# Kernel tuning notes

Measured on AMD Instinct MI355X. Metric: run time of the kernel, lower is better.

## Reference

```python
import jax, jax.numpy as jnp
import numpy as np

D_MODEL = 1024
N_LAYER = 2
VOCAB = 32000
D_STATE = 16
D_INNER = 2048  # expand * d_model
DT_RANK = 64    # ceil(d_model / 16)
D_CONV = 4
B, L = 2, 1024


def setup_inputs() -> dict:
    key = jax.random.key(0)
    ks = jax.random.split(key, 8)
    s = lambda k, shape, scale=0.02: (jax.random.normal(k, shape, jnp.float32) * scale)
    return {
        "input_ids": jax.random.randint(ks[0], (B, L), 0, VOCAB),
        "emb": s(ks[1], (VOCAB, D_MODEL)),
        "norm_f_w": jnp.ones((D_MODEL,), jnp.float32),
        "W_in_l": s(ks[2], (N_LAYER, D_INNER, D_MODEL)),
        "W_in_r": s(ks[3], (N_LAYER, D_INNER, D_MODEL)),
        "conv_w": s(ks[4], (N_LAYER, D_INNER, D_CONV), 0.1),
        "conv_b": jnp.zeros((N_LAYER, D_INNER), jnp.float32),
        "W_x": s(ks[5], (N_LAYER, DT_RANK + 2 * D_STATE, D_INNER)),
        "W_dt": s(ks[6], (N_LAYER, D_INNER, DT_RANK)),
        "A_log": jnp.log(jnp.broadcast_to(jnp.arange(1, D_STATE + 1, dtype=jnp.float32), (N_LAYER, D_INNER, D_STATE))),
        "Dp": jnp.ones((N_LAYER, D_INNER), jnp.float32),
        "W_out": s(ks[7], (N_LAYER, D_MODEL, D_INNER)),
        "norm_w": jnp.ones((N_LAYER, D_MODEL), jnp.float32),
    }


def _rmsnorm(x, w, eps=1e-5):
    return x * jax.lax.rsqrt(jnp.mean(x * x, axis=-1, keepdims=True) + eps) * w


def _silu(x):
    return x * jax.nn.sigmoid(x)


def _selective_scan(u, delta, A, Bm, Cm, Dv):
    # u, delta: [b,l,d]; A: [d,n]; Bm, Cm: [b,l,n]; Dv: [d]
    deltaA = jnp.exp(jnp.einsum('bld,dn->bldn', delta, A))          # [b,l,d,n]
    deltaB_u = (delta * u)[..., None] * Bm[:, :, None, :]            # [b,l,d,n]

    def step(carry, inp):
        dA_t, dBu_t, C_t = inp                 # [b,d,n],[b,d,n],[b,n]
        x = dA_t * carry + dBu_t
        y = jnp.einsum('bdn,bn->bd', x, C_t)
        return x, y

    b, l, d = u.shape
    n = A.shape[1]
    x0 = jnp.zeros((b, d, n), u.dtype)
    xs = (jnp.swapaxes(deltaA, 0, 1), jnp.swapaxes(deltaB_u, 0, 1), jnp.swapaxes(Cm, 0, 1))
    _, ys = jax.lax.scan(step, x0, xs)         # ys: [l,b,d]
    return jnp.swapaxes(ys, 0, 1) + u * Dv


def _mamba_block(x, Wl, Wr, cw, cb, Wx, Wdt, Alog, Dv, Wo):
    b, l, _ = x.shape
    res = x @ Wr.T                              # [b,l,di]
    xi = x @ Wl.T                               # [b,l,di]
    # depthwise causal conv over length (torch pads d_conv-1 both sides then slices [:l])
    xt = jnp.swapaxes(xi, 1, 2)                 # [b,di,l]
    xc = jax.lax.conv_general_dilated(
        xt, cw[:, None, :], window_strides=(1,), padding=[(D_CONV - 1, 0)],
        dimension_numbers=('NCH', 'OIH', 'NCH'), feature_group_count=D_INNER)
    xc = xc + cb[None, :, None]
    u = _silu(jnp.swapaxes(xc, 1, 2))           # [b,l,di]
    x_dbl = u @ Wx.T                            # [b,l,dt_rank+2n]
    dlt = x_dbl[..., :DT_RANK]
    Bm = x_dbl[..., DT_RANK:DT_RANK + D_STATE]
    Cm = x_dbl[..., DT_RANK + D_STATE:]
    delta = jax.nn.softplus(dlt @ Wdt.T)        # [b,l,di]
    A = -jnp.exp(Alog)
    y = _selective_scan(u, delta, A, Bm, Cm, Dv)
    y = y * _silu(res)
    return y @ Wo.T


def reference(input_ids, emb, norm_f_w, W_in_l, W_in_r, conv_w, conv_b, W_x, W_dt, A_log, Dp, W_out, norm_w):
    x = emb[input_ids]                          # [b,l,d_model]
    for i in range(N_LAYER):
        x = _mamba_block(_rmsnorm(x, norm_w[i]), W_in_l[i], W_in_r[i], conv_w[i], conv_b[i],
                         W_x[i], W_dt[i], A_log[i], Dp[i], W_out[i]) + x
    x = _rmsnorm(x, norm_f_w)
    return x @ emb.T                            # tied lm_head: [b,l,vocab]
```

## Files before the change

### kernel.cpp

```cpp
#include <hip/hip_runtime.h>
#include <math.h>

#define D_MODEL 1024
#define N_LAYER 2
#define VOCAB   32000
#define D_STATE 16
#define D_INNER 2048
#define DT_RANK 64
#define D_CONV  4
#define BB      2
#define LL      1024
#define TT      (BB*LL)
#define XLD     (2*D_INNER)

typedef __attribute__((ext_vector_type(8))) short bf16x8;
typedef __attribute__((ext_vector_type(4))) float f32x4;

static __device__ __forceinline__ unsigned short bfr(float f) {
  unsigned int u = __float_as_uint(f);
  return (unsigned short)((u + 0x7FFFu + ((u >> 16) & 1u)) >> 16);
}
static __device__ __forceinline__ float b2f(unsigned short h) {
  return __uint_as_float((unsigned int)h << 16);
}
static __device__ __forceinline__ unsigned int pack2(float a, float b) {
  return (unsigned int)bfr(a) | ((unsigned int)bfr(b) << 16);
}

template<int CTRL>
static __device__ __forceinline__ float dpp_sum_step(float x) {
  int v = __builtin_amdgcn_update_dpp(0, __float_as_int(x), CTRL, 0xF, 0xF, false);
  return x + __int_as_float(v);
}

static __device__ __forceinline__ void gload16(const void* g, void* l) {
  __builtin_amdgcn_global_load_lds(
      (const __attribute__((address_space(1))) void*)g,
      (__attribute__((address_space(3))) void*)l, 16, 0, 0);
}

__global__ __launch_bounds__(256) void embed_kernel(
    const int* __restrict__ ids, const float* __restrict__ emb,
    float* __restrict__ x) {
  int t  = blockIdx.x;
  int id = ids[t];
  const float4* src = (const float4*)(emb + (size_t)id * D_MODEL);
  float4*       dst = (float4*)(x + (size_t)t * D_MODEL);
  dst[threadIdx.x] = src[threadIdx.x];
}

__global__ __launch_bounds__(256) void rmsnorm_bf_kernel(
    const float* __restrict__ x, const float* __restrict__ w,
    unsigned short* __restrict__ o) {
  int t = blockIdx.x;
  const float4* xr = (const float4*)(x + (size_t)t * D_MODEL);
  float4 v = xr[threadIdx.x];
  float ss = v.x*v.x + v.y*v.y + v.z*v.z + v.w*v.w;
  for (int off = 32; off > 0; off >>= 1) ss += __shfl_down(ss, off, 64);
  __shared__ float wsum[4];
  if ((threadIdx.x & 63) == 0) wsum[threadIdx.x >> 6] = ss;
  __syncthreads();
  float tot = wsum[0] + wsum[1] + wsum[2] + wsum[3];
  float scale = rsqrtf(tot / (float)D_MODEL + 1e-5f);
  float4 wv = ((const float4*)w)[threadIdx.x];
  ushort4 ov;
  ov.x = bfr(v.x * scale * wv.x);
  ov.y = bfr(v.y * scale * wv.y);
  ov.z = bfr(v.z * scale * wv.z);
  ov.w = bfr(v.w * scale * wv.w);
  ((ushort4*)(o + (size_t)t * D_MODEL))[threadIdx.x] = ov;
}

__global__ __launch_bounds__(256) void cvt_bf_kernel(
    const float* __restrict__ s, unsigned short* __restrict__ d, int n8) {
  int i = blockIdx.x * 256 + threadIdx.x;
  if (i >= n8) return;
  const float4* p = (const float4*)s + (size_t)i * 2;
  float4 a = p[0], b = p[1];
  uint4 o;
  o.x = pack2(a.x, a.y); o.y = pack2(a.z, a.w);
  o.z = pack2(b.x, b.y); o.w = pack2(b.z, b.w);
  ((uint4*)d)[i] = o;
}

__global__ __launch_bounds__(256) void cvt_dlt_kernel(
    const float* __restrict__ xdbl, unsigned short* __restrict__ d) {
  int i = blockIdx.x * 256 + threadIdx.x;
  int t = i >> 3, j8 = (i & 7) * 8;
  const float4* p = (const float4*)(xdbl + (size_t)t * 128 + j8);
  float4 a = p[0], b = p[1];
  uint4 o;
  o.x = pack2(a.x, a.y); o.y = pack2(a.z, a.w);
  o.z = pack2(b.x, b.y); o.w = pack2(b.z, b.w);
  *(uint4*)(d + (size_t)t * 64 + j8) = o;
}

__global__ __launch_bounds__(256) void zero_kernel(float* __restrict__ p) {
  ((float4*)p)[blockIdx.x * 256 + threadIdx.x] = make_float4(0.f, 0.f, 0.f, 0.f);
}

#define GBM 128
#define GBN 128
#define GBK 32
#define LDK 40

template<bool BF>
static __device__ __forceinline__ void stage8(short* dst, const void* src, int ld,
                                              int grow, int gcol, bool valid) {
  uint4 w = make_uint4(0u, 0u, 0u, 0u);
  if (valid) {
    if constexpr (BF) {
      w = *(const uint4*)((const unsigned short*)src + (size_t)grow * ld + gcol);
    } else {
      const float* p = (const float*)src + (size_t)grow * ld + gcol;
      float4 v0 = *(const float4*)p;
      float4 v1 = *(const float4*)(p + 4);
      w.x = pack2(v0.x, v0.y); w.y = pack2(v0.z, v0.w);
      w.z = pack2(v1.x, v1.y); w.w = pack2(v1.z, v1.w);
    }
  }
  *(uint4*)dst = w;
}

template<bool ABF, bool BBF, bool RESID>
__global__ __launch_bounds__(256) void gemm_mfma(
    const void* __restrict__ Av, int lda,
    const void* __restrict__ Bv, int ldb,
    float* __restrict__ C, int ldc,
    int N, int K, const float* __restrict__ resid) {
  __shared__ short As[GBM * LDK];
  __shared__ short Bs[GBN * LDK];
  const int tid  = threadIdx.x;
  const int lane = tid & 63;
  const int wid  = tid >> 6;
  const int wm   = (wid >> 1) * 64;
  const int wn   = (wid & 1) * 64;
  const int bm   = blockIdx.y * GBM;
  const int bn   = blockIdx.x * GBN;

  f32x4 acc[4][4] = {};

  const int r0 = tid >> 2;
  const int cg = (tid & 3) * 8;
  const int fm = wm + (lane & 15);
  const int fn = wn + (lane & 15);
  const int fk = (lane >> 4) * 8;

  for (int k0 = 0; k0 < K; k0 += GBK) {
    stage8<ABF>(&As[(size_t)r0 * LDK + cg],        Av, lda, bm + r0,      k0 + cg, true);
    stage8<ABF>(&As[(size_t)(r0 + 64) * LDK + cg], Av, lda, bm + r0 + 64, k0 + cg, true);
    stage8<BBF>(&Bs[(size_t)r0 * LDK + cg],        Bv, ldb, bn + r0,      k0 + cg, (bn + r0) < N);
    stage8<BBF>(&Bs[(size_t)(r0 + 64) * LDK + cg], Bv, ldb, bn + r0 + 64, k0 + cg, (bn + r0 + 64) < N);
    __syncthreads();

    bf16x8 aq[4], bq[4];
#pragma unroll
    for (int i = 0; i < 4; i++) aq[i] = *(const bf16x8*)&As[(size_t)(fm + 16 * i) * LDK + fk];
#pragma unroll
    for (int i = 0; i < 4; i++) bq[i] = *(const bf16x8*)&Bs[(size_t)(fn + 16 * i) * LDK + fk];
#pragma unroll
    for (int mt = 0; mt < 4; mt++)
#pragma unroll
      for (int nt = 0; nt < 4; nt++)
        acc[mt][nt] = __builtin_amdgcn_mfma_f32_16x16x32_bf16(
            aq[mt], bq[nt], acc[mt][nt], 0, 0, 0);
    __syncthreads();
  }

  const int col   = lane & 15;
  const int rbase = (lane >> 4) * 4;
#pragma unroll
  for (int mt = 0; mt < 4; mt++) {
#pragma unroll
    for (int nt = 0; nt < 4; nt++) {
      int gn = bn + wn + nt * 16 + col;
      if (gn < N) {
        int gm = bm + wm + mt * 16 + rbase;
#pragma unroll
        for (int i = 0; i < 4; i++) {
          size_t o = (size_t)(gm + i) * ldc + gn;
          float r = RESID ? resid[o] : 0.f;
          C[o] = acc[mt][nt][i] + r;
        }
      }
    }
  }
}

#define NBM 128
#define NBN 128
#define NBK 64

template<bool ATOMIC>
__global__ __launch_bounds__(256) void gemm_bf(
    const unsigned short* __restrict__ A, int lda,
    const unsigned short* __restrict__ B, int ldb,
    float* __restrict__ C, int ldc,
    int N, int kc, int gx, int nwg) {
  __shared__ short As[NBM * NBK];
  __shared__ short Bs[NBN * NBK];
  const int tid  = threadIdx.x;
  const int lane = tid & 63;
  const int wid  = tid >> 6;
  const int wm   = (wid >> 1) * 64;
  const int wn   = (wid & 1) * 64;

  const int lin = blockIdx.y * gx + blockIdx.x;
  const int swz = (lin & 7) * (nwg >> 3) + (lin >> 3);
  const int bm  = (swz % gx) * NBM;
  const int bn  = (swz / gx) * NBN;
  const int kb  = blockIdx.z * kc;

  const int sr  = tid >> 3;
  const int scl = 8 * ((tid & 7) ^ (sr & 7));
  const unsigned short* pA[4];
  const unsigned short* pB[4];
#pragma unroll
  for (int i = 0; i < 4; i++) {
    pA[i] = A + (size_t)(bm + sr + 32 * i) * lda + kb + scl;
    int rb = bn + sr + 32 * i; if (rb >= N) rb = N - 1;
    pB[i] = B + (size_t)rb * ldb + kb + scl;
  }
  short* lA = As + tid * 8;
  short* lB = Bs + tid * 8;

  f32x4 acc[4][4] = {};
  const int fr = lane & 15;
  const int fs = lane >> 4;

  for (int k0 = 0; k0 < kc; k0 += NBK) {
#pragma unroll
    for (int i = 0; i < 4; i++) gload16(pA[i], lA + i * 2048);
#pragma unroll
    for (int i = 0; i < 4; i++) gload16(pB[i], lB + i * 2048);
    __syncthreads();

    bf16x8 aq[2][4], bq[2][4];
#pragma unroll
    for (int kk = 0; kk < 2; kk++) {
#pragma unroll
      for (int i = 0; i < 4; i++) {
        int ra = wm + 16 * i + fr;
        aq[kk][i] = *(const bf16x8*)&As[ra * 64 + 8 * ((kk * 4 + fs) ^ (ra & 7))];
        int rb = wn + 16 * i + fr;
        bq[kk][i] = *(const bf16x8*)&Bs[rb * 64 + 8 * ((kk * 4 + fs) ^ (rb & 7))];
      }
    }
#pragma unroll
    for (int kk = 0; kk < 2; kk++)
#pragma unroll
      for (int mt = 0; mt < 4; mt++)
#pragma unroll
        for (int nt = 0; nt < 4; nt++)
          acc[mt][nt] = __builtin_amdgcn_mfma_f32_16x16x32_bf16(
              aq[kk][mt], bq[kk][nt], acc[mt][nt], 0, 0, 0);
    __syncthreads();
#pragma unroll
    for (int i = 0; i < 4; i++) { pA[i] += NBK; pB[i] += NBK; }
  }

  const int col   = lane & 15;
  const int rbase = (lane >> 4) * 4;
#pragma unroll
  for (int mt = 0; mt < 4; mt++) {
#pragma unroll
    for (int nt = 0; nt < 4; nt++) {
      int gn = bn + wn + nt * 16 + col;
      if (gn < N) {
        int gm = bm + wm + mt * 16 + rbase;
#pragma unroll
        for (int i = 0; i < 4; i++) {
          size_t o = (size_t)(gm + i) * ldc + gn;
          if constexpr (ATOMIC) atomicAdd(&C[o], acc[mt][nt][i]);
          else                  C[o] = acc[mt][nt][i];
        }
      }
    }
  }
}

__global__ __launch_bounds__(256) void conv_silu_kernel(
    const float* __restrict__ xires, const float* __restrict__ cw,
    const float* __restrict__ cb, unsigned short* __restrict__ u) {
  size_t idx = (size_t)blockIdx.x * 256 + threadIdx.x;
  int j = (int)(idx & (D_INNER - 1));
  int t = (int)(idx >> 11);
  int b = t >> 10;
  int l = t & (LL - 1);
  float acc = cb[j];
#pragma unroll
  for (int k = 0; k < D_CONV; k++) {
    int ls = l - (D_CONV - 1) + k;
    if (ls >= 0)
      acc += xires[((size_t)b * LL + ls) * XLD + j] * cw[j * D_CONV + k];
  }
  float sig = 1.f / (1.f + __expf(-acc));
  u[idx] = bfr(acc * sig);
}

#define CT 64
#define NC (LL / CT)

__global__ __launch_bounds__(256) void scan_kernel(
    const float* __restrict__ xires,
    const unsigned short* __restrict__ ub,
    const float* __restrict__ xdbl,
    const float* __restrict__ Alog,
    const float* __restrict__ Dp,
    unsigned short* __restrict__ yg) {
  const int tid = threadIdx.x;
  const int d0  = blockIdx.x * 16;
  const int b   = blockIdx.y;
  const int dl  = tid >> 4;
  const int n   = tid & 15;
  const int tq  = tid >> 2;
  const int jq  = tid & 3;

  __shared__ float4 sc[2][CT][17];
  __shared__ float2 bcs[2][CT][17];

  const float a = -__expf(Alog[(size_t)(d0 + dl) * D_STATE + n]);
  const float4 Dv4 = *(const float4*)(Dp + d0 + jq * 4);
  const float* Dvp = (const float*)&Dv4;

  const size_t bt = (size_t)b * LL;
  float st = 0.f;
  unsigned short* outp = yg + bt * D_INNER + d0 + dl;

  auto loadc = [&](int c, float4& xi4, float4& rs4, ushort4& u4,
                   float4& B4, float4& C4) {
    size_t r = bt + (size_t)c * CT + tq;
    const float* row = xires + r * XLD + d0 + jq * 4;
    xi4 = *(const float4*)row;
    rs4 = *(const float4*)(row + D_INNER);
    u4  = *(const ushort4*)(ub  + r * D_INNER + d0 + jq * 4);
    B4  = *(const float4*)(xdbl + r * 128 + 64 + jq * 4);
    C4  = *(const float4*)(xdbl + r * 128 + 80 + jq * 4);
  };
  auto xform = [&](int bw, float4 xi4, float4 rs4, ushort4 u4,
                   float4 B4, float4 C4) {
    const float* xp = (const float*)&xi4;
    const float* rp = (const float*)&rs4;
    const unsigned short* up = (const unsigned short*)&u4;
    const float* Bp = (const float*)&B4;
    const float* Cp = (const float*)&C4;
#pragma unroll
    for (int j = 0; j < 4; j++) {
      float dr = xp[j], rv = rp[j], uv = b2f(up[j]);
      float dlt = fmaxf(dr, 0.f) + log1pf(__expf(-fabsf(dr)));
      float g   = rv / (1.f + __expf(-rv));
      float4 s;
      s.x = dlt; s.y = dlt * uv; s.z = g; s.w = uv * Dvp[j] * g;
      sc[bw][tq][jq * 4 + j] = s;
      float2 w; w.x = Bp[j]; w.y = Cp[j];
      bcs[bw][tq][jq * 4 + j] = w;
    }
  };

  {
    float4 xi4, rs4, B4, C4; ushort4 u4;
    loadc(0, xi4, rs4, u4, B4, C4);
    xform(0, xi4, rs4, u4, B4, C4);
  }
  __syncthreads();

  int buf = 0;
  for (int c = 0; c < NC; c++) {
    float4 xi4, rs4, B4, C4; ushort4 u4;
    const bool pf = (c + 1 < NC);
    if (pf) loadc(c + 1, xi4, rs4, u4, B4, C4);

#pragma unroll 8
    for (int t = 0; t < CT; t++) {
      float4 s = sc[buf][t][dl];
      float2 w = bcs[buf][t][n];
      float e  = __expf(s.x * a);
      st = fmaf(e, st, s.y * w.x);
      float yp = st * w.y;
      yp = dpp_sum_step<0x111>(yp);
      yp = dpp_sum_step<0x112>(yp);
      yp = dpp_sum_step<0x114>(yp);
      yp = dpp_sum_step<0x118>(yp);
      if (n == 15)
        outp[(size_t)(c * CT + t) * D_INNER] = bfr(fmaf(yp, s.z, s.w));
    }

    if (pf) xform(buf ^ 1, xi4, rs4, u4, B4, C4);
    __syncthreads();
    buf ^= 1;
  }
}

extern "C" void kernel_launch(void* const* d_in, const int* in_sizes, int n_in,
                              void* d_out, int out_size, void* d_ws, size_t ws_size,
                              hipStream_t stream) {
  const int*   ids    = (const int*)  d_in[0];
  const float* emb    = (const float*)d_in[1];
  const float* normfw = (const float*)d_in[2];
  const float* Winl   = (const float*)d_in[3];
  const float* Winr   = (const float*)d_in[4];
  const float* convw  = (const float*)d_in[5];
  const float* convb  = (const float*)d_in[6];
  const float* Wx     = (const float*)d_in[7];
  const float* Wdt    = (const float*)d_in[8];
  const float* Alog   = (const float*)d_in[9];
  const float* Dp     = (const float*)d_in[10];
  const float* Wout   = (const float*)d_in[11];
  const float* normw  = (const float*)d_in[12];
  float* out = (float*)d_out;

  float* x    = (float*)d_ws;
  float* xi   = x    + (size_t)TT * D_MODEL;
  float* res  = xi   + (size_t)TT * D_INNER;
  float* xdbl = res  + (size_t)TT * D_INNER;
  unsigned short* xn_bf = (unsigned short*)(xdbl + (size_t)TT * 128);
  unsigned short* u_bf  = xn_bf + (size_t)TT * D_MODEL;
  unsigned short* yg_bf = u_bf  + (size_t)TT * D_INNER;
  unsigned short* dlt_bf = yg_bf  + (size_t)TT * D_INNER;
  unsigned short* emb_bf = dlt_bf + (size_t)TT * DT_RANK;
  unsigned short* wlr_bf = emb_bf + (size_t)VOCAB * D_MODEL;
  unsigned short* wx_bf  = wlr_bf + (size_t)N_LAYER * 2 * D_INNER * D_MODEL;
  unsigned short* wdt_bf = wx_bf  + (size_t)N_LAYER * (DT_RANK + 2*D_STATE) * D_INNER;
  unsigned short* wout_bf= wdt_bf + (size_t)N_LAYER * D_INNER * DT_RANK;
  const size_t NEED = (size_t)((char*)(wout_bf + (size_t)N_LAYER * D_MODEL * D_INNER) - (char*)d_ws);
  const bool big = ws_size >= NEED;

  float* xires = xi;

  embed_kernel<<<TT, 256, 0, stream>>>(ids, emb, x);

  if (big) {
    cvt_bf_kernel<<<(VOCAB*D_MODEL/8 + 255)/256, 256, 0, stream>>>(emb, emb_bf, VOCAB*D_MODEL/8);
    for (int i = 0; i < N_LAYER; i++) {
      unsigned short* dst = wlr_bf + (size_t)i * 2 * D_INNER * D_MODEL;
      cvt_bf_kernel<<<(D_INNER*D_MODEL/8 + 255)/256, 256, 0, stream>>>(
          Winl + (size_t)i * D_INNER * D_MODEL, dst, D_INNER*D_MODEL/8);
      cvt_bf_kernel<<<(D_INNER*D_MODEL/8 + 255)/256, 256, 0, stream>>>(
          Winr + (size_t)i * D_INNER * D_MODEL, dst + (size_t)D_INNER*D_MODEL, D_INNER*D_MODEL/8);
    }
    cvt_bf_kernel<<<(N_LAYER*96*D_INNER/8 + 255)/256, 256, 0, stream>>>(Wx, wx_bf, N_LAYER*96*D_INNER/8);
    cvt_bf_kernel<<<(N_LAYER*D_INNER*DT_RANK/8 + 255)/256, 256, 0, stream>>>(Wdt, wdt_bf, N_LAYER*D_INNER*DT_RANK/8);
    cvt_bf_kernel<<<(N_LAYER*D_MODEL*D_INNER/8 + 255)/256, 256, 0, stream>>>(Wout, wout_bf, N_LAYER*D_MODEL*D_INNER/8);

    for (int i = 0; i < N_LAYER; i++) {
      const unsigned short* wlr = wlr_bf + (size_t)i * 2 * D_INNER * D_MODEL;
      const unsigned short* wx  = wx_bf  + (size_t)i * 96 * D_INNER;
      const unsigned short* wdt = wdt_bf + (size_t)i * D_INNER * DT_RANK;
      const unsigned short* wo  = wout_bf+ (size_t)i * D_MODEL * D_INNER;
      const float* cw  = convw + (size_t)i * D_INNER * D_CONV;
      const float* cb  = convb + (size_t)i * D_INNER;
      const float* Al  = Alog  + (size_t)i * D_INNER * D_STATE;
      const float* Dpl = Dp    + (size_t)i * D_INNER;
      const float* nw  = normw + (size_t)i * D_MODEL;

      rmsnorm_bf_kernel<<<TT, 256, 0, stream>>>(x, nw, xn_bf);
      gemm_bf<false><<<dim3(TT/NBM, XLD/NBN), 256, 0, stream>>>(
          xn_bf, D_MODEL, wlr, D_MODEL, xires, XLD, XLD, D_MODEL,
          TT/NBM, (TT/NBM)*(XLD/NBN));
      conv_silu_kernel<<<(TT * D_INNER) / 256, 256, 0, stream>>>(xires, cw, cb, u_bf);
      zero_kernel<<<(TT * 128 / 4) / 256, 256, 0, stream>>>(xdbl);
      gemm_bf<true><<<dim3(TT/NBM, 1, 16), 256, 0, stream>>>(
          u_bf, D_INNER, wx, D_INNER, xdbl, 128, 96, D_INNER / 16,
          TT/NBM, TT/NBM);
      cvt_dlt_kernel<<<(TT * 8) / 256, 256, 0, stream>>>(xdbl, dlt_bf);
      gemm_bf<false><<<dim3(TT/NBM, D_INNER/NBN), 256, 0, stream>>>(
          dlt_bf, DT_RANK, wdt, DT_RANK, xires, XLD, D_INNER, DT_RANK,
          TT/NBM, (TT/NBM)*(D_INNER/NBN));
      scan_kernel<<<dim3(D_INNER/16, BB), 256, 0, stream>>>(
          xires, u_bf, xdbl, Al, Dpl, yg_bf);
      gemm_bf<true><<<dim3(TT/NBM, D_MODEL/NBN, 4), 256, 0, stream>>>(
          yg_bf, D_INNER, wo, D_INNER, x, D_MODEL, D_MODEL, D_INNER / 4,
          TT/NBM, (TT/NBM)*(D_MODEL/NBN));
    }

    rmsnorm_bf_kernel<<<TT, 256, 0, stream>>>(x, normfw, xn_bf);
    gemm_bf<false><<<dim3(TT/NBM, VOCAB/NBN), 256, 0, stream>>>(
        xn_bf, D_MODEL, emb_bf, D_MODEL, out, VOCAB, VOCAB, D_MODEL,
        TT/NBM, (TT/NBM)*(VOCAB/NBN));
    return;
  }

  for (int i = 0; i < N_LAYER; i++) {
    const float* Wl  = Winl  + (size_t)i * D_INNER * D_MODEL;
    const float* Wr  = Winr  + (size_t)i * D_INNER * D_MODEL;
    const float* cw  = convw + (size_t)i * D_INNER * D_CONV;
    const float* cb  = convb + (size_t)i * D_INNER;
    const float* Wxl = Wx    + (size_t)i * (DT_RANK + 2*D_STATE) * D_INNER;
    const float* Wdl = Wdt   + (size_t)i * D_INNER * DT_RANK;
    const float* Al  = Alog  + (size_t)i * D_INNER * D_STATE;
    const float* Dpl = Dp    + (size_t)i * D_INNER;
    const float* Wo  = Wout  + (size_t)i * D_MODEL * D_INNER;
    const float* nw  = normw + (size_t)i * D_MODEL;

    rmsnorm_bf_kernel<<<TT, 256, 0, stream>>>(x, nw, xn_bf);
    gemm_mfma<true, false, false><<<dim3(D_INNER/GBN, TT/GBM), 256, 0, stream>>>(
        xn_bf, D_MODEL, Wl, D_MODEL, xi, D_INNER, D_INNER, D_MODEL, nullptr);
    gemm_mfma<true, false, false><<<dim3(D_INNER/GBN, TT/GBM), 256, 0, stream>>>(
        xn_bf, D_MODEL, Wr, D_MODEL, res, D_INNER, D_INNER, D_MODEL, nullptr);
    {
    }
    conv_silu_kernel<<<(TT * D_INNER) / 256, 256, 0, stream>>>(
        xi, cw, cb, u_bf);
    gemm_mfma<true, false, false><<<dim3(1, TT/GBM), 256, 0, stream>>>(
        u_bf, D_INNER, Wxl, D_INNER, xdbl, 128, DT_RANK + 2*D_STATE, D_INNER, nullptr);
    gemm_mfma<false, false, false><<<dim3(D_INNER/GBN, TT/GBM), 256, 0, stream>>>(
        xdbl, 128, Wdl, DT_RANK, xi, D_INNER, D_INNER, DT_RANK, nullptr);
    scan_kernel<<<dim3(D_INNER/16, BB), 256, 0, stream>>>(
        xi, u_bf, xdbl, Al, Dpl, yg_bf);
    gemm_mfma<true, false, true><<<dim3(D_MODEL/GBN, TT/GBM), 256, 0, stream>>>(
        yg_bf, D_INNER, Wo, D_INNER, x, D_MODEL, D_MODEL, D_INNER, x);
  }

  rmsnorm_bf_kernel<<<TT, 256, 0, stream>>>(x, normfw, xn_bf);
  gemm_mfma<true, false, false><<<dim3(VOCAB/GBN, TT/GBM), 256, 0, stream>>>(
      xn_bf, D_MODEL, emb, D_MODEL, out, VOCAB, VOCAB, D_MODEL, nullptr);
}
```

Before: 1.148 ms.

## Replace atomic split-K with partial buffers plus reduce kernels; tile conv over time

Split-K GEMMs for x_dbl and the output projection now write per-slice partial results into a scratch buffer (aliased onto the logits output) instead of atomically adding. Separate reduction kernels then sum the slices: one also converts the delta columns to bf16, which removes the zero and convert kernels, and the other adds the residual. The conv+SiLU kernel processes four timesteps per thread so neighbouring inputs are loaded once and reused. The tile swizzle is dropped, which may hurt L2 locality, and the partial buffers add extra memory traffic.

```diff
diff --git a/kernel.cpp b/kernel.cpp
--- a/kernel.cpp
+++ b/kernel.cpp
@@ -83,20 +83,34 @@
   ((uint4*)d)[i] = o;
 }
 
-__global__ __launch_bounds__(256) void cvt_dlt_kernel(
-    const float* __restrict__ xdbl, unsigned short* __restrict__ d) {
-  int i = blockIdx.x * 256 + threadIdx.x;
-  int t = i >> 3, j8 = (i & 7) * 8;
-  const float4* p = (const float4*)(xdbl + (size_t)t * 128 + j8);
-  float4 a = p[0], b = p[1];
-  uint4 o;
-  o.x = pack2(a.x, a.y); o.y = pack2(a.z, a.w);
-  o.z = pack2(b.x, b.y); o.w = pack2(b.z, b.w);
-  *(uint4*)(d + (size_t)t * 64 + j8) = o;
-}
-
-__global__ __launch_bounds__(256) void zero_kernel(float* __restrict__ p) {
-  ((float4*)p)[blockIdx.x * 256 + threadIdx.x] = make_float4(0.f, 0.f, 0.f, 0.f);
+__global__ __launch_bounds__(256) void reduce_xdbl_kernel(
+    const float* __restrict__ parts, float* __restrict__ xdbl,
+    unsigned short* __restrict__ dlt) {
+  int idx = blockIdx.x * 256 + threadIdx.x;
+  float4 s = make_float4(0.f, 0.f, 0.f, 0.f);
+#pragma unroll
+  for (int z = 0; z < 16; z++) {
+    float4 v = ((const float4*)parts)[(size_t)z * (TT * 32) + idx];
+    s.x += v.x; s.y += v.y; s.z += v.z; s.w += v.w;
+  }
+  ((float4*)xdbl)[idx] = s;
+  int t = idx >> 5, q = idx & 31;
+  if (q < 16) {
+    uint2 o; o.x = pack2(s.x, s.y); o.y = pack2(s.z, s.w);
+    *(uint2*)(dlt + (size_t)t * 64 + q * 4) = o;
+  }
+}
+
+__global__ __launch_bounds__(256) void reduce_wo_kernel(
+    const float* __restrict__ parts, float* __restrict__ x) {
+  int idx = blockIdx.x * 256 + threadIdx.x;
+  float4 s = ((float4*)x)[idx];
+#pragma unroll
+  for (int z = 0; z < 4; z++) {
+    float4 v = ((const float4*)parts)[(size_t)z * (TT * 256) + idx];
+    s.x += v.x; s.y += v.y; s.z += v.z; s.w += v.w;
+  }
+  ((float4*)x)[idx] = s;
 }
 
 #define GBM 128
@@ -191,12 +205,11 @@
 #define NBN 128
 #define NBK 64
 
-template<bool ATOMIC>
 __global__ __launch_bounds__(256) void gemm_bf(
     const unsigned short* __restrict__ A, int lda,
     const unsigned short* __restrict__ B, int ldb,
     float* __restrict__ C, int ldc,
-    int N, int kc, int gx, int nwg) {
+    int N, int kc, size_t partStride) {
   __shared__ short As[NBM * NBK];
   __shared__ short Bs[NBN * NBK];
   const int tid  = threadIdx.x;
@@ -204,12 +217,10 @@
   const int wid  = tid >> 6;
   const int wm   = (wid >> 1) * 64;
   const int wn   = (wid & 1) * 64;
-
-  const int lin = blockIdx.y * gx + blockIdx.x;
-  const int swz = (lin & 7) * (nwg >> 3) + (lin >> 3);
-  const int bm  = (swz % gx) * NBM;
-  const int bn  = (swz / gx) * NBN;
-  const int kb  = blockIdx.z * kc;
+  const int bm   = blockIdx.x * NBM;
+  const int bn   = blockIdx.y * NBN;
+  const int kb   = blockIdx.z * kc;
+  float* Cp      = C + (size_t)blockIdx.z * partStride;
 
   const int sr  = tid >> 3;
   const int scl = 8 * ((tid & 7) ^ (sr & 7));
@@ -253,7 +264,7 @@
 #pragma unroll
         for (int nt = 0; nt < 4; nt++)
           acc[mt][nt] = __builtin_amdgcn_mfma_f32_16x16x32_bf16(
-              aq[kk][mt], bq[kk][nt], acc[mt][nt], 0, 0, 0);
+              aq[kk][mt], bq[kk][nt], acc[kk ? mt : mt][nt], 0, 0, 0);
     __syncthreads();
 #pragma unroll
     for (int i = 0; i < 4; i++) { pA[i] += NBK; pB[i] += NBK; }
@@ -271,8 +282,7 @@
 #pragma unroll
         for (int i = 0; i < 4; i++) {
           size_t o = (size_t)(gm + i) * ldc + gn;
-          if constexpr (ATOMIC) atomicAdd(&C[o], acc[mt][nt][i]);
-          else                  C[o] = acc[mt][nt][i];
+          Cp[o] = acc[mt][nt][i];
         }
       }
     }
@@ -282,20 +292,28 @@
 __global__ __launch_bounds__(256) void conv_silu_kernel(
     const float* __restrict__ xires, const float* __restrict__ cw,
     const float* __restrict__ cb, unsigned short* __restrict__ u) {
-  size_t idx = (size_t)blockIdx.x * 256 + threadIdx.x;
-  int j = (int)(idx & (D_INNER - 1));
-  int t = (int)(idx >> 11);
-  int b = t >> 10;
-  int l = t & (LL - 1);
-  float acc = cb[j];
-#pragma unroll
-  for (int k = 0; k < D_CONV; k++) {
-    int ls = l - (D_CONV - 1) + k;
-    if (ls >= 0)
-      acc += xires[((size_t)b * LL + ls) * XLD + j] * cw[j * D_CONV + k];
-  }
-  float sig = 1.f / (1.f + __expf(-acc));
-  u[idx] = bfr(acc * sig);
+  int idx = blockIdx.x * 256 + threadIdx.x;
+  int j  = idx & (D_INNER - 1);
+  int g  = idx >> 11;
+  int b  = g >> 8;
+  int l0 = (g & 255) * 4;
+  float w0 = cw[j * D_CONV + 0], w1 = cw[j * D_CONV + 1];
+  float w2 = cw[j * D_CONV + 2], w3 = cw[j * D_CONV + 3];
+  float bias = cb[j];
+  const float* base = xires + ((size_t)b * LL) * XLD + j;
+  float v[7];
+#pragma unroll
+  for (int dl = 0; dl < 7; dl++) {
+    int ls = l0 - 3 + dl;
+    v[dl] = (ls >= 0) ? base[(size_t)ls * XLD] : 0.f;
+  }
+  unsigned short* up = u + ((size_t)b * LL + l0) * D_INNER + j;
+#pragma unroll
+  for (int t = 0; t < 4; t++) {
+    float acc = bias + v[t] * w0 + v[t+1] * w1 + v[t+2] * w2 + v[t+3] * w3;
+    float sig = 1.f / (1.f + __expf(-acc));
+    up[(size_t)t * D_INNER] = bfr(acc * sig);
+  }
 }
 
 #define CT 64
@@ -426,6 +444,7 @@
   const bool big = ws_size >= NEED;
 
   float* xires = xi;
+  float* parts = out;
 
   embed_kernel<<<TT, 256, 0, stream>>>(ids, emb, x);
 
@@ -454,59 +473,52 @@
       const float* nw  = normw + (size_t)i * D_MODEL;
 
       rmsnorm_bf_kernel<<<TT, 256, 0, stream>>>(x, nw, xn_bf);
-      gemm_bf<false><<<dim3(TT/NBM, XLD/NBN), 256, 0, stream>>>(
-          xn_bf, D_MODEL, wlr, D_MODEL, xires, XLD, XLD, D_MODEL,
-          TT/NBM, (TT/NBM)*(XLD/NBN));
-      conv_silu_kernel<<<(TT * D_INNER) / 256, 256, 0, stream>>>(xires, cw, cb, u_bf);
-      zero_kernel<<<(TT * 128 / 4) / 256, 256, 0, stream>>>(xdbl);
-      gemm_bf<true><<<dim3(TT/NBM, 1, 16), 256, 0, stream>>>(
-          u_bf, D_INNER, wx, D_INNER, xdbl, 128, 96, D_INNER / 16,
-          TT/NBM, TT/NBM);
-      cvt_dlt_kernel<<<(TT * 8) / 256, 256, 0, stream>>>(xdbl, dlt_bf);
-      gemm_bf<false><<<dim3(TT/NBM, D_INNER/NBN), 256, 0, stream>>>(
-          dlt_bf, DT_RANK, wdt, DT_RANK, xires, XLD, D_INNER, DT_RANK,
-          TT/NBM, (TT/NBM)*(D_INNER/NBN));
+      gemm_bf<<<dim3(TT/NBM, XLD/NBN), 256, 0, stream>>>(
+          xn_bf, D_MODEL, wlr, D_MODEL, xires, XLD, XLD, D_MODEL, 0);
+      conv_silu_kernel<<<(TT/4) * D_INNER / 256, 256, 0, stream>>>(xires, cw, cb, u_bf);
+      gemm_bf<<<dim3(TT/NBM, 1, 16), 256, 0, stream>>>(
+          u_bf, D_INNER, wx, D_INNER, parts, 128, 96, D_INNER / 16, (size_t)TT * 128);
+      reduce_xdbl_kernel<<<(TT * 32) / 256, 256, 0, stream>>>(parts, xdbl, dlt_bf);
+      gemm_bf<<<dim3(TT/NBM, D_INNER/NBN), 256, 0, stream>>>(
+          dlt_bf, DT_RANK, wdt, DT_RANK, xires, XLD, D_INNER, DT_RANK, 0);
       scan_kernel<<<dim3(D_INNER/16, BB), 256, 0, stream>>>(
           xires, u_bf, xdbl, Al, Dpl, yg_bf);
-      gemm_bf<true><<<dim3(TT/NBM, D_MODEL/NBN, 4), 256, 0, stream>>>(
-          yg_bf, D_INNER, wo, D_INNER, x, D_MODEL, D_MODEL, D_INNER / 4,
-          TT/NBM, (TT/NBM)*(D_MODEL/NBN));
+      gemm_bf<<<dim3(TT/NBM, D_MODEL/NBN, 4), 256, 0, stream>>>(
+          yg_bf, D_INNER, wo, D_INNER, parts, D_MODEL, D_MODEL, D_INNER / 4,
+          (size_t)TT * D_MODEL);
+      reduce_wo_kernel<<<(TT * 256) / 256, 256, 0, stream>>>(parts, x);
     }
 
     rmsnorm_bf_kernel<<<TT, 256, 0, stream>>>(x, normfw, xn_bf);
-    gemm_bf<false><<<dim3(TT/NBM, VOCAB/NBN), 256, 0, stream>>>(
-        xn_bf, D_MODEL, emb_bf, D_MODEL, out, VOCAB, VOCAB, D_MODEL,
-        TT/NBM, (TT/NBM)*(VOCAB/NBN));
+    gemm_bf<<<dim3(TT/NBM, VOCAB/NBN), 256, 0, stream>>>(
+        xn_bf, D_MODEL, emb_bf, D_MODEL, out, VOCAB, VOCAB, D_MODEL, 0);
     return;
   }
 
   for (int i = 0; i < N_LAYER; i++) {
     const float* Wl  = Winl  + (size_t)i * D_INNER * D_MODEL;
     const float* Wr  = Winr  + (size_t)i * D_INNER * D_MODEL;
-    const float* cw  = convw + (size_t)i * D_INNER * D_CONV;
-    const float* cb  = convb + (size_t)i * D_INNER;
     const float* Wxl = Wx    + (size_t)i * (DT_RANK + 2*D_STATE) * D_INNER;
     const float* Wdl = Wdt   + (size_t)i * D_INNER * DT_RANK;
     const float* Al  = Alog  + (size_t)i * D_INNER * D_STATE;
     const float* Dpl = Dp    + (size_t)i * D_INNER;
     const float* Wo  = Wout  + (size_t)i * D_MODEL * D_INNER;
+    const float* cw  = convw + (size_t)i * D_INNER * D_CONV;
+    const float* cb  = convb + (size_t)i * D_INNER;
     const float* nw  = normw + (size_t)i * D_MODEL;
 
     rmsnorm_bf_kernel<<<TT, 256, 0, stream>>>(x, nw, xn_bf);
-    gemm_mfma<true, false, false><<<dim3(D_INNER/GBN, TT/GBM), 256, 0, stream>>>(
-        xn_bf, D_MODEL, Wl, D_MODEL, xi, D_INNER, D_INNER, D_MODEL, nullptr);
-    gemm_mfma<true, false, false><<<dim3(D_INNER/GBN, TT/GBM), 256, 0, stream>>>(
-        xn_bf, D_MODEL, Wr, D_MODEL, res, D_INNER, D_INNER, D_MODEL, nullptr);
-    {
-    }
-    conv_silu_kernel<<<(TT * D_INNER) / 256, 256, 0, stream>>>(
-        xi, cw, cb, u_bf);
+    gemm_mfma<true, false, false><<<dim3(XLD/GBN, TT/GBM), 256, 0, stream>>>(
+        xn_bf, D_MODEL, Wl, D_MODEL, xires, XLD, D_INNER, D_MODEL, nullptr);
+    gemm_mfma<true, false, false><<<dim3(XLD/GBN, TT/GBM), 256, 0, stream>>>(
+        xn_bf, D_MODEL, Wr, D_MODEL, xires + D_INNER, XLD, D_INNER, D_MODEL, nullptr);
+    conv_silu_kernel<<<(TT/4) * D_INNER / 256, 256, 0, stream>>>(xires, cw, cb, u_bf);
     gemm_mfma<true, false, false><<<dim3(1, TT/GBM), 256, 0, stream>>>(
         u_bf, D_INNER, Wxl, D_INNER, xdbl, 128, DT_RANK + 2*D_STATE, D_INNER, nullptr);
-    gemm_mfma<false, false, false><<<dim3(D_INNER/GBN, TT/GBM), 256, 0, stream>>>(
-        xdbl, 128, Wdl, DT_RANK, xi, D_INNER, D_INNER, DT_RANK, nullptr);
+    gemm_mfma<false, false, false><<<dim3(XLD/GBN, TT/GBM), 256, 0, stream>>>(
+        xdbl, 128, Wdl, DT_RANK, xires, XLD, D_INNER, DT_RANK, nullptr);
     scan_kernel<<<dim3(D_INNER/16, BB), 256, 0, stream>>>(
-        xi, u_bf, xdbl, Al, Dpl, yg_bf);
+        xires, u_bf, xdbl, Al, Dpl, yg_bf);
     gemm_mfma<true, false, true><<<dim3(D_MODEL/GBN, TT/GBM), 256, 0, stream>>>(
         yg_bf, D_INNER, Wo, D_INNER, x, D_MODEL, D_MODEL, D_INNER, x);
   }
```

Result: faster. 1.072 ms (-6.6%).
